# Optimization experiments

Hardware: AMD Instinct MI355X
Metric: run time of the kernel (lower is better)

Reference implementation:

```python
import jax, jax.numpy as jnp
import numpy as np

HEADS = 8
FEATURE = 512
COMPUTE = 256
SEQ = 512
BATCH = 64


def setup_inputs() -> dict:
    key = jax.random.key(0)
    ks = jax.random.split(key, 10)
    d1 = jax.random.normal(ks[0], (BATCH, FEATURE), dtype=jnp.float32)
    d2 = jax.random.normal(ks[1], (SEQ, BATCH, FEATURE), dtype=jnp.float32)
    # linear1: Linear(FEATURE -> COMPUTE) + ReLU
    w1 = jax.random.normal(ks[2], (FEATURE, COMPUTE), dtype=jnp.float32) * (1.0 / np.sqrt(FEATURE))
    b1 = jnp.zeros((COMPUTE,), dtype=jnp.float32)
    # per-head score params, stacked: ws[i] is [2C, C], ps[i] is [C, 1]
    W = jax.random.normal(ks[3], (HEADS, 2 * COMPUTE, COMPUTE), dtype=jnp.float32)
    P = jax.random.normal(ks[4], (HEADS, COMPUTE), dtype=jnp.float32)
    # value projection weight_v: [FEATURE, COMPUTE]
    wv = jax.random.normal(ks[5], (FEATURE, COMPUTE), dtype=jnp.float32)
    # cc: Linear(COMPUTE*HEADS -> 128) + ReLU
    wcc = jax.random.normal(ks[6], (COMPUTE * HEADS, 128), dtype=jnp.float32) * (1.0 / np.sqrt(COMPUTE * HEADS))
    bcc = jnp.zeros((128,), dtype=jnp.float32)
    return {"d1": d1, "d2": d2, "w1": w1, "b1": b1, "W": W, "P": P,
            "wv": wv, "wcc": wcc, "bcc": bcc, "d2_size": SEQ}


def reference(d1, d2, w1, b1, W, P, wv, wcc, bcc, d2_size):
    S, B, F = d2.shape
    # linear1 on flattened d2 rows -> [S*B, C]
    d3 = jax.nn.relu(d2.reshape(-1, F) @ w1 + b1)
    # linear1 on d1, tiled S times along batch axis -> [S*B, C]
    d4 = jax.nn.relu(d1 @ w1 + b1)            # [B, C]
    d4 = jnp.tile(d4, (S, 1))                  # [S*B, C]
    d5 = jnp.concatenate([d3, d4], axis=1).reshape(S, B, -1)  # [S, B, 2C]
    # value path: tanh(d2 @ weight_v) -> [B, S, C]
    tv = jnp.tanh(jnp.einsum('sbf,fc->sbc', d2, wv)).transpose(1, 0, 2)
    # all heads batched: us = tanh(d5 @ W_h) -> [H, S, B, C]
    us = jnp.tanh(jnp.einsum('sbd,hdc->hsbc', d5, W))
    atts = jnp.einsum('hsbc,hc->hbs', us, P)   # [H, B, S]
    scores = jax.nn.softmax(atts, axis=-1)     # softmax over sequence
    vs = jnp.einsum('hbs,bsc->hbc', scores, tv)  # weighted sum over S -> [H, B, C]
    # torch.cat(vs, dim=1): head-major concat -> [B, H*C]
    vs = vs.transpose(1, 0, 2).reshape(B, -1)
    return jax.nn.relu(vs @ wcc + bcc)         # [B, 128]
```

## Files before the change

kernel.cpp:

```cpp
#include <hip/hip_runtime.h>
#include <cstddef>
#include <cstdint>

#define HH 8
#define FF 512
#define CC 256
#define SS 512
#define BB 64
#define SB (SS*BB)

typedef __attribute__((ext_vector_type(4))) float f32x4;
typedef __attribute__((ext_vector_type(8))) short bf16x8;

__device__ __forceinline__ float fast_tanh(float x) {
    float e = __expf(2.0f * x);
    return 1.0f - 2.0f / (e + 1.0f);
}
__device__ __forceinline__ float relu_f(float x) { return fmaxf(x, 0.0f); }

__device__ __forceinline__ unsigned short f2bf(float x) {
    unsigned u = __float_as_uint(x);
    unsigned r = u + 0x7FFFu + ((u >> 16) & 1u);
    return (unsigned short)(r >> 16);
}
__device__ __forceinline__ float bf2f(unsigned short h) {
    return __uint_as_float(((unsigned)h) << 16);
}

__global__ __launch_bounds__(256) void p_prep(
    const float* __restrict__ w1, const float* __restrict__ wv,
    const float* __restrict__ W, const float* __restrict__ d1,
    const float* __restrict__ b1,
    unsigned short* __restrict__ w1t_hi, unsigned short* __restrict__ w1t_lo,
    unsigned short* __restrict__ wvt_hi, unsigned short* __restrict__ wvt_lo,
    unsigned short* __restrict__ Wt_hi, unsigned short* __restrict__ Wt_lo,
    float* __restrict__ d4)
{
    __shared__ float T[64][65];
    __shared__ float As[16][68];
    __shared__ float Bs[16][68];
    const int tid = threadIdx.x;
    const int bid = blockIdx.x;
    if (bid < 192) {
        const float* src;
        unsigned short *dhi, *dlo;
        int K, kt, nt;
        if (bid < 64) {
            int m = bid >> 5;
            int t = bid & 31;
            kt = t >> 2; nt = t & 3; K = FF;
            src = m ? wv : w1;
            dhi = m ? wvt_hi : w1t_hi;
            dlo = m ? wvt_lo : w1t_lo;
        } else {
            int t = bid - 64;
            int h = t >> 4; int tt = t & 15;
            kt = tt >> 2; nt = tt & 3; K = CC;
            src = W + (size_t)h * 2 * CC * CC;
            dhi = Wt_hi + (size_t)h * CC * CC;
            dlo = Wt_lo + (size_t)h * CC * CC;
        }
        const int k0 = kt * 64, n0 = nt * 64;
        #pragma unroll
        for (int jj = 0; jj < 4; ++jj) {
            int i = (tid >> 4) + jj * 16;
            int j = (tid & 15) * 4;
            float4 v = *(const float4*)(src + (size_t)(k0 + i) * CC + n0 + j);
            T[i][j] = v.x; T[i][j+1] = v.y; T[i][j+2] = v.z; T[i][j+3] = v.w;
        }
        __syncthreads();
        #pragma unroll
        for (int jj = 0; jj < 4; ++jj) {
            int n = (tid >> 4) + jj * 16;
            int kq = (tid & 15) * 4;
            unsigned short hv[4], lv[4];
            #pragma unroll
            for (int q = 0; q < 4; ++q) {
                float x = T[kq + q][n];
                unsigned short hx = f2bf(x);
                hv[q] = hx; lv[q] = f2bf(x - bf2f(hx));
            }
            size_t o = (size_t)(n0 + n) * K + k0 + kq;
            *(ushort4*)(dhi + o) = *(ushort4*)hv;
            *(ushort4*)(dlo + o) = *(ushort4*)lv;
        }
    } else {
        const int n0 = (bid - 192) * 64;
        const int tx = tid & 15, ty = tid >> 4;
        const int lm = tid >> 2, lk4 = (tid & 3) * 4;
        const int bk = tid >> 4, bn4 = (tid & 15) * 4;
        float acc[4][4] = {};
        for (int k0 = 0; k0 < FF; k0 += 16) {
            float4 a = *(const float4*)(d1 + (size_t)lm * FF + k0 + lk4);
            As[lk4+0][lm] = a.x; As[lk4+1][lm] = a.y;
            As[lk4+2][lm] = a.z; As[lk4+3][lm] = a.w;
            *(float4*)&Bs[bk][bn4] = *(const float4*)(w1 + (size_t)(k0+bk)*CC + n0 + bn4);
            __syncthreads();
            #pragma unroll
            for (int kk = 0; kk < 16; ++kk) {
                float4 a4 = *(const float4*)&As[kk][ty*4];
                float4 b4 = *(const float4*)&Bs[kk][tx*4];
                float av[4] = {a4.x, a4.y, a4.z, a4.w};
                float bv[4] = {b4.x, b4.y, b4.z, b4.w};
                #pragma unroll
                for (int i = 0; i < 4; ++i)
                    #pragma unroll
                    for (int j = 0; j < 4; ++j)
                        acc[i][j] = fmaf(av[i], bv[j], acc[i][j]);
            }
            __syncthreads();
        }
        #pragma unroll
        for (int i = 0; i < 4; ++i) {
            int row = ty*4 + i;
            #pragma unroll
            for (int j = 0; j < 4; ++j)
                d4[(size_t)row*CC + n0 + tx*4 + j] = relu_f(acc[i][j] + b1[n0 + tx*4 + j]);
        }
    }
}

__global__ __launch_bounds__(256, 2) void k1_main(
    const float* __restrict__ d2,
    const unsigned short* __restrict__ w1t_hi, const unsigned short* __restrict__ w1t_lo,
    const unsigned short* __restrict__ wvt_hi, const unsigned short* __restrict__ wvt_lo,
    const float* __restrict__ b1,
    const float* __restrict__ d4, const float* __restrict__ W,
    unsigned short* __restrict__ d3_hi, unsigned short* __restrict__ d3_lo,
    unsigned short* __restrict__ tv, float* __restrict__ e4)
{
    __shared__ __align__(16) unsigned short A_hi[128][40];
    __shared__ __align__(16) unsigned short A_lo[128][40];
    __shared__ __align__(16) unsigned short B_hi[256][40];
    __shared__ __align__(16) unsigned short B_lo[256][40];

    const int tid = threadIdx.x;
    const int bid = blockIdx.x;

    if (bid >= 512) {
        float (*As)[68] = (float(*)[68])&A_hi[0][0];
        float (*Bs)[68] = (float(*)[68])&A_lo[0][0];
        const int idx = bid - 512;
        const int n0 = (idx & 3) * 64;
        const int h  = idx >> 2;
        const float* Wh = W + ((size_t)h * 2 * CC + CC) * CC;
        const int tx = tid & 15, ty = tid >> 4;
        const int lm = tid >> 2, lk4 = (tid & 3) * 4;
        const int bk = tid >> 4, bn4 = (tid & 15) * 4;
        float acc[4][4] = {};
        for (int k0 = 0; k0 < CC; k0 += 16) {
            float4 a = *(const float4*)(d4 + (size_t)lm * CC + k0 + lk4);
            As[lk4+0][lm] = a.x; As[lk4+1][lm] = a.y;
            As[lk4+2][lm] = a.z; As[lk4+3][lm] = a.w;
            *(float4*)&Bs[bk][bn4] = *(const float4*)(Wh + (size_t)(k0+bk)*CC + n0 + bn4);
            __syncthreads();
            #pragma unroll
            for (int kk = 0; kk < 16; ++kk) {
                float4 a4 = *(const float4*)&As[kk][ty*4];
                float4 b4 = *(const float4*)&Bs[kk][tx*4];
                float av[4] = {a4.x, a4.y, a4.z, a4.w};
                float bv[4] = {b4.x, b4.y, b4.z, b4.w};
                #pragma unroll
                for (int i = 0; i < 4; ++i)
                    #pragma unroll
                    for (int j = 0; j < 4; ++j)
                        acc[i][j] = fmaf(av[i], bv[j], acc[i][j]);
            }
            __syncthreads();
        }
        #pragma unroll
        for (int i = 0; i < 4; ++i) {
            int b = ty*4 + i;
            #pragma unroll
            for (int j = 0; j < 4; ++j)
                e4[((size_t)h*BB + b)*CC + n0 + tx*4 + j] = acc[i][j];
        }
        return;
    }

    const int path = bid >> 8;
    const int r0 = (bid & 255) * 128;
    const int lane = tid & 63, w = tid >> 6;
    const int rowgrp = w & 1, colgrp = w >> 1;
    const int cb = lane & 15, quad = lane >> 4;
    const unsigned short* BH = path ? wvt_hi : w1t_hi;
    const unsigned short* BL = path ? wvt_lo : w1t_lo;

    f32x4 acc[4][8];
    f32x4 zero = {0.0f, 0.0f, 0.0f, 0.0f};
    #pragma unroll
    for (int rt = 0; rt < 4; ++rt)
        #pragma unroll
        for (int ct = 0; ct < 8; ++ct) acc[rt][ct] = zero;

    const int ar = tid >> 1, ak = (tid & 1) * 16;

    for (int k0 = 0; k0 < FF; k0 += 32) {
        {
            const float* src = d2 + (size_t)(r0 + ar) * FF + k0 + ak;
            float v[16];
            *(float4*)&v[0]  = *(const float4*)(src);
            *(float4*)&v[4]  = *(const float4*)(src + 4);
            *(float4*)&v[8]  = *(const float4*)(src + 8);
            *(float4*)&v[12] = *(const float4*)(src + 12);
            bf16x8 vh0, vh1, vl0, vl1;
            #pragma unroll
            for (int j = 0; j < 8; ++j) {
                unsigned short h = f2bf(v[j]);
                vh0[j] = (short)h; vl0[j] = (short)f2bf(v[j] - bf2f(h));
                unsigned short h2 = f2bf(v[j+8]);
                vh1[j] = (short)h2; vl1[j] = (short)f2bf(v[j+8] - bf2f(h2));
            }
            *(bf16x8*)&A_hi[ar][ak]     = vh0;
            *(bf16x8*)&A_hi[ar][ak + 8] = vh1;
            *(bf16x8*)&A_lo[ar][ak]     = vl0;
            *(bf16x8*)&A_lo[ar][ak + 8] = vl1;
        }
        #pragma unroll
        for (int j = 0; j < 4; ++j) {
            int idx = j * 256 + tid;
            int n = idx >> 2, kp = (idx & 3) * 8;
            *(bf16x8*)&B_hi[n][kp] = *(const bf16x8*)(BH + (size_t)n * FF + k0 + kp);
            *(bf16x8*)&B_lo[n][kp] = *(const bf16x8*)(BL + (size_t)n * FF + k0 + kp);
        }
        __syncthreads();
        bf16x8 ahf[4], alf[4];
        #pragma unroll
        for (int rt = 0; rt < 4; ++rt) {
            ahf[rt] = *(bf16x8*)&A_hi[rowgrp*64 + rt*16 + cb][quad*8];
            alf[rt] = *(bf16x8*)&A_lo[rowgrp*64 + rt*16 + cb][quad*8];
        }
        #pragma unroll
        for (int ct = 0; ct < 8; ++ct) {
            bf16x8 bh = *(bf16x8*)&B_hi[colgrp*128 + ct*16 + cb][quad*8];
            bf16x8 bl = *(bf16x8*)&B_lo[colgrp*128 + ct*16 + cb][quad*8];
            #pragma unroll
            for (int rt = 0; rt < 4; ++rt) {
                acc[rt][ct] = __builtin_amdgcn_mfma_f32_16x16x32_bf16(ahf[rt], bh, acc[rt][ct], 0, 0, 0);
                acc[rt][ct] = __builtin_amdgcn_mfma_f32_16x16x32_bf16(ahf[rt], bl, acc[rt][ct], 0, 0, 0);
                acc[rt][ct] = __builtin_amdgcn_mfma_f32_16x16x32_bf16(alf[rt], bh, acc[rt][ct], 0, 0, 0);
            }
        }
        __syncthreads();
    }
    if (path == 0) {
        float bias[8];
        #pragma unroll
        for (int ct = 0; ct < 8; ++ct) bias[ct] = b1[colgrp*128 + ct*16 + cb];
        #pragma unroll
        for (int rt = 0; rt < 4; ++rt) {
            #pragma unroll
            for (int r = 0; r < 4; ++r) {
                int gr = r0 + rowgrp*64 + rt*16 + quad*4 + r;
                #pragma unroll
                for (int ct = 0; ct < 8; ++ct) {
                    int c = colgrp*128 + ct*16 + cb;
                    float val = relu_f(acc[rt][ct][r] + bias[ct]);
                    unsigned short hv = f2bf(val);
                    d3_hi[(size_t)gr * CC + c] = hv;
                    d3_lo[(size_t)gr * CC + c] = f2bf(val - bf2f(hv));
                }
            }
        }
    } else {
        #pragma unroll
        for (int rt = 0; rt < 4; ++rt) {
            #pragma unroll
            for (int r = 0; r < 4; ++r) {
                int gr = r0 + rowgrp*64 + rt*16 + quad*4 + r;
                int s = gr >> 6, b = gr & 63;
                #pragma unroll
                for (int ct = 0; ct < 8; ++ct) {
                    int c = colgrp*128 + ct*16 + cb;
                    tv[((size_t)b * SS + s) * CC + c] = f2bf(fast_tanh(acc[rt][ct][r]));
                }
            }
        }
    }
}

__global__ __launch_bounds__(256, 2) void k3_atts(
    const unsigned short* __restrict__ d3_hi, const unsigned short* __restrict__ d3_lo,
    const unsigned short* __restrict__ Wt_hi, const unsigned short* __restrict__ Wt_lo,
    const float* __restrict__ e4, const float* __restrict__ P,
    float* __restrict__ atts)
{
    __shared__ __align__(16) unsigned short A_hi[128][40];
    __shared__ __align__(16) unsigned short A_lo[128][40];
    __shared__ __align__(16) unsigned short B_hi[256][40];
    __shared__ __align__(16) unsigned short B_lo[256][40];
    __shared__ float red[2][128];

    const int tid = threadIdx.x;
    const int lane = tid & 63, w = tid >> 6;
    const int h = blockIdx.y;
    const int r0 = blockIdx.x * 128;
    const int rowgrp = w & 1, colgrp = w >> 1;
    const int cb = lane & 15, quad = lane >> 4;

    const unsigned short* WhH = Wt_hi + (size_t)h * CC * CC;
    const unsigned short* WhL = Wt_lo + (size_t)h * CC * CC;

    f32x4 acc[4][8];
    f32x4 zero = {0.0f, 0.0f, 0.0f, 0.0f};
    #pragma unroll
    for (int rt = 0; rt < 4; ++rt)
        #pragma unroll
        for (int ct = 0; ct < 8; ++ct) acc[rt][ct] = zero;

    const int ar = tid >> 1, ak = (tid & 1) * 16;

    for (int k0 = 0; k0 < CC; k0 += 32) {
        *(bf16x8*)&A_hi[ar][ak]     = *(const bf16x8*)(d3_hi + (size_t)(r0 + ar) * CC + k0 + ak);
        *(bf16x8*)&A_hi[ar][ak + 8] = *(const bf16x8*)(d3_hi + (size_t)(r0 + ar) * CC + k0 + ak + 8);
        *(bf16x8*)&A_lo[ar][ak]     = *(const bf16x8*)(d3_lo + (size_t)(r0 + ar) * CC + k0 + ak);
        *(bf16x8*)&A_lo[ar][ak + 8] = *(const bf16x8*)(d3_lo + (size_t)(r0 + ar) * CC + k0 + ak + 8);
        #pragma unroll
        for (int j = 0; j < 4; ++j) {
            int idx = j * 256 + tid;
            int n = idx >> 2, kp = (idx & 3) * 8;
            *(bf16x8*)&B_hi[n][kp] = *(const bf16x8*)(WhH + (size_t)n * CC + k0 + kp);
            *(bf16x8*)&B_lo[n][kp] = *(const bf16x8*)(WhL + (size_t)n * CC + k0 + kp);
        }
        __syncthreads();
        bf16x8 ahf[4], alf[4];
        #pragma unroll
        for (int rt = 0; rt < 4; ++rt) {
            ahf[rt] = *(bf16x8*)&A_hi[rowgrp*64 + rt*16 + cb][quad*8];
            alf[rt] = *(bf16x8*)&A_lo[rowgrp*64 + rt*16 + cb][quad*8];
        }
        #pragma unroll
        for (int ct = 0; ct < 8; ++ct) {
            bf16x8 bh = *(bf16x8*)&B_hi[colgrp*128 + ct*16 + cb][quad*8];
            bf16x8 bl = *(bf16x8*)&B_lo[colgrp*128 + ct*16 + cb][quad*8];
            #pragma unroll
            for (int rt = 0; rt < 4; ++rt) {
                acc[rt][ct] = __builtin_amdgcn_mfma_f32_16x16x32_bf16(ahf[rt], bh, acc[rt][ct], 0, 0, 0);
                acc[rt][ct] = __builtin_amdgcn_mfma_f32_16x16x32_bf16(ahf[rt], bl, acc[rt][ct], 0, 0, 0);
                acc[rt][ct] = __builtin_amdgcn_mfma_f32_16x16x32_bf16(alf[rt], bh, acc[rt][ct], 0, 0, 0);
            }
        }
        __syncthreads();
    }
    float Pv[8];
    #pragma unroll
    for (int ct = 0; ct < 8; ++ct) Pv[ct] = P[(size_t)h * CC + colgrp*128 + ct*16 + cb];
    #pragma unroll
    for (int rt = 0; rt < 4; ++rt) {
        #pragma unroll
        for (int r = 0; r < 4; ++r) {
            int b = rt*16 + quad*4 + r;
            const float* e4p = e4 + ((size_t)h * BB + b) * CC + colgrp*128 + cb;
            float part = 0.0f;
            #pragma unroll
            for (int ct = 0; ct < 8; ++ct) {
                float u = acc[rt][ct][r] + e4p[ct*16];
                part = fmaf(Pv[ct], fast_tanh(u), part);
            }
            part += __shfl_xor(part, 1); part += __shfl_xor(part, 2);
            part += __shfl_xor(part, 4); part += __shfl_xor(part, 8);
            if (cb == 0) red[colgrp][rowgrp*64 + b] = part;
        }
    }
    __syncthreads();
    if (tid < 128) {
        float v = red[0][tid] + red[1][tid];
        int gr = r0 + tid;
        int s = gr >> 6, b = gr & 63;
        atts[((size_t)h * BB + b) * SS + s] = v;
    }
}

__global__ __launch_bounds__(256) void k456_out(
    const float* __restrict__ atts, const unsigned short* __restrict__ tv,
    const float* __restrict__ wcc, const float* __restrict__ bcc,
    float* __restrict__ out)
{
    __shared__ float sc[HH][SS];
    __shared__ float red[4][2048];
    const int b = blockIdx.x;
    const int tid = threadIdx.x;
    const int lane = tid & 63, w = tid >> 6;

    for (int i = tid; i < HH*SS; i += 256) {
        int h = i >> 9, s = i & 511;
        sc[h][s] = atts[((size_t)h*BB + b)*SS + s];
    }
    __syncthreads();
    #pragma unroll
    for (int t = 0; t < 2; ++t) {
        int hh = w*2 + t;
        float x[8];
        #pragma unroll
        for (int j = 0; j < 8; ++j) x[j] = sc[hh][j*64 + lane];
        float m = x[0];
        #pragma unroll
        for (int j = 1; j < 8; ++j) m = fmaxf(m, x[j]);
        #pragma unroll
        for (int d = 1; d < 64; d <<= 1) m = fmaxf(m, __shfl_xor(m, d));
        float sum = 0.0f;
        #pragma unroll
        for (int j = 0; j < 8; ++j) { x[j] = __expf(x[j] - m); sum += x[j]; }
        #pragma unroll
        for (int d = 1; d < 64; d <<= 1) sum += __shfl_xor(sum, d);
        float inv = 1.0f / sum;
        #pragma unroll
        for (int j = 0; j < 8; ++j) sc[hh][j*64 + lane] = x[j] * inv;
    }
    __syncthreads();
    {
        const int cl = tid & 63, stripe = tid >> 6;
        const int c0 = cl * 4;
        const unsigned short* tvb = tv + ((size_t)b * SS + stripe * 128) * CC + c0;
        float acc[HH][4] = {};
        for (int si = 0; si < 128; ++si) {
            uint2 u = *(const uint2*)(tvb + (size_t)si * CC);
            float x0 = bf2f((unsigned short)(u.x));
            float x1 = bf2f((unsigned short)(u.x >> 16));
            float x2 = bf2f((unsigned short)(u.y));
            float x3 = bf2f((unsigned short)(u.y >> 16));
            int s = stripe * 128 + si;
            #pragma unroll
            for (int h = 0; h < HH; ++h) {
                float wgt = sc[h][s];
                acc[h][0] = fmaf(wgt, x0, acc[h][0]);
                acc[h][1] = fmaf(wgt, x1, acc[h][1]);
                acc[h][2] = fmaf(wgt, x2, acc[h][2]);
                acc[h][3] = fmaf(wgt, x3, acc[h][3]);
            }
        }
        #pragma unroll
        for (int h = 0; h < HH; ++h)
            #pragma unroll
            for (int j = 0; j < 4; ++j)
                red[stripe][h*256 + c0 + j] = acc[h][j];
    }
    __syncthreads();
    for (int i = tid; i < 2048; i += 256)
        red[0][i] = red[0][i] + red[1][i] + red[2][i] + red[3][i];
    __syncthreads();
    {
        const int n = tid & 127, half = tid >> 7;
        float o = 0.0f;
        const int kbase = half * 1024;
        for (int k = 0; k < 1024; ++k)
            o = fmaf(red[0][kbase + k], wcc[(size_t)(kbase + k) * 128 + n], o);
        float* r2 = &sc[0][0];
        r2[half * 128 + n] = o;
    }
    __syncthreads();
    if (tid < 128)
        out[(size_t)b * 128 + tid] = relu_f(sc[0][tid] + sc[0][128 + tid] + bcc[tid]);
}

extern "C" void kernel_launch(void* const* d_in, const int* in_sizes, int n_in,
                              void* d_out, int out_size, void* d_ws, size_t ws_size,
                              hipStream_t stream)
{
    (void)in_sizes; (void)n_in; (void)out_size; (void)ws_size;
    const float* d1  = (const float*)d_in[0];
    const float* d2  = (const float*)d_in[1];
    const float* w1  = (const float*)d_in[2];
    const float* b1  = (const float*)d_in[3];
    const float* W   = (const float*)d_in[4];
    const float* P   = (const float*)d_in[5];
    const float* wv  = (const float*)d_in[6];
    const float* wcc = (const float*)d_in[7];
    const float* bcc = (const float*)d_in[8];
    float* out = (float*)d_out;

    char* p = (char*)d_ws;
    unsigned short* d3_hi = (unsigned short*)p;  p += (size_t)SB * CC * 2;
    unsigned short* d3_lo = (unsigned short*)p;  p += (size_t)SB * CC * 2;
    unsigned short* tv    = (unsigned short*)p;  p += (size_t)BB * SS * CC * 2;
    unsigned short* w1t_hi = (unsigned short*)p; p += (size_t)CC * FF * 2;
    unsigned short* w1t_lo = (unsigned short*)p; p += (size_t)CC * FF * 2;
    unsigned short* wvt_hi = (unsigned short*)p; p += (size_t)CC * FF * 2;
    unsigned short* wvt_lo = (unsigned short*)p; p += (size_t)CC * FF * 2;
    unsigned short* Wt_hi  = (unsigned short*)p; p += (size_t)HH * CC * CC * 2;
    unsigned short* Wt_lo  = (unsigned short*)p; p += (size_t)HH * CC * CC * 2;
    float* d4   = (float*)p;  p += (size_t)BB * CC * 4;
    float* e4   = (float*)p;  p += (size_t)HH * BB * CC * 4;
    float* atts = (float*)p;  p += (size_t)HH * BB * SS * 4;

    p_prep   <<<dim3(196),       256, 0, stream>>>(w1, wv, W, d1, b1,
                  w1t_hi, w1t_lo, wvt_hi, wvt_lo, Wt_hi, Wt_lo, d4);
    k1_main  <<<dim3(544),       256, 0, stream>>>(d2, w1t_hi, w1t_lo,
                  wvt_hi, wvt_lo, b1, d4, W, d3_hi, d3_lo, tv, e4);
    k3_atts  <<<dim3(256, HH),   256, 0, stream>>>(d3_hi, d3_lo, Wt_hi, Wt_lo,
                  e4, P, atts);
    k456_out <<<dim3(BB),        256, 0, stream>>>(atts, tv, wcc, bcc, out);
}
```

Baseline: 370.2 us.

## Load weight tiles via async global-to-LDS and A fragments directly into registers

In both GEMM kernels the B (weight) tiles are now copied with global_load_lds, which goes straight from global memory into LDS without passing through registers. The LDS rows are unpadded, 32 elements wide. The A operand is no longer staged in LDS: each wave loads its MFMA fragments directly from global memory, and in k1 also converts them to hi/lo bf16 there. This cuts LDS traffic and footprint, and may raise occupancy. The cost is that unpadded B rows can cause LDS bank conflicts on the fragment reads, and A rows are re-read by the two column-group waves.

Result: slower. 406.3 us (+9.7%).

```diff
diff --git a/kernel.cpp b/kernel.cpp
--- a/kernel.cpp
+++ b/kernel.cpp
@@ -25,6 +25,13 @@
 }
 __device__ __forceinline__ float bf2f(unsigned short h) {
     return __uint_as_float(((unsigned)h) << 16);
+}
+
+__device__ __forceinline__ void async16(void* lds, const void* gp) {
+    __builtin_amdgcn_global_load_lds(
+        (const __attribute__((address_space(1))) unsigned int*)gp,
+        (__attribute__((address_space(3))) unsigned int*)lds,
+        16, 0, 0);
 }
 
 __global__ __launch_bounds__(256) void p_prep(
@@ -129,17 +136,15 @@
     unsigned short* __restrict__ d3_hi, unsigned short* __restrict__ d3_lo,
     unsigned short* __restrict__ tv, float* __restrict__ e4)
 {
-    __shared__ __align__(16) unsigned short A_hi[128][40];
-    __shared__ __align__(16) unsigned short A_lo[128][40];
-    __shared__ __align__(16) unsigned short B_hi[256][40];
-    __shared__ __align__(16) unsigned short B_lo[256][40];
+    __shared__ __align__(16) unsigned short B_hi[256][32];
+    __shared__ __align__(16) unsigned short B_lo[256][32];
+    __shared__ float As[16][68];
+    __shared__ float Bs[16][68];
 
     const int tid = threadIdx.x;
     const int bid = blockIdx.x;
 
     if (bid >= 512) {
-        float (*As)[68] = (float(*)[68])&A_hi[0][0];
-        float (*Bs)[68] = (float(*)[68])&A_lo[0][0];
         const int idx = bid - 512;
         const int n0 = (idx & 3) * 64;
         const int h  = idx >> 2;
@@ -186,6 +191,9 @@
     const unsigned short* BH = path ? wvt_hi : w1t_hi;
     const unsigned short* BL = path ? wvt_lo : w1t_lo;
 
+    const int dn = w * 64 + (lane >> 2);
+    const int dk = (lane & 3) * 8;
+
     f32x4 acc[4][8];
     f32x4 zero = {0.0f, 0.0f, 0.0f, 0.0f};
     #pragma unroll
@@ -193,43 +201,28 @@
         #pragma unroll
         for (int ct = 0; ct < 8; ++ct) acc[rt][ct] = zero;
 
-    const int ar = tid >> 1, ak = (tid & 1) * 16;
-
     for (int k0 = 0; k0 < FF; k0 += 32) {
-        {
-            const float* src = d2 + (size_t)(r0 + ar) * FF + k0 + ak;
-            float v[16];
-            *(float4*)&v[0]  = *(const float4*)(src);
-            *(float4*)&v[4]  = *(const float4*)(src + 4);
-            *(float4*)&v[8]  = *(const float4*)(src + 8);
-            *(float4*)&v[12] = *(const float4*)(src + 12);
-            bf16x8 vh0, vh1, vl0, vl1;
+        #pragma unroll
+        for (int jj = 0; jj < 4; ++jj) {
+            const size_t go = (size_t)(dn + jj*16) * FF + k0 + dk;
+            async16((char*)B_hi + (w*4 + jj) * 1024, BH + go);
+            async16((char*)B_lo + (w*4 + jj) * 1024, BL + go);
+        }
+        bf16x8 ahf[4], alf[4];
+        #pragma unroll
+        for (int rt = 0; rt < 4; ++rt) {
+            const float* ap = d2 + (size_t)(r0 + rowgrp*64 + rt*16 + cb) * FF + k0 + quad*8;
+            float v[8];
+            *(float4*)&v[0] = *(const float4*)ap;
+            *(float4*)&v[4] = *(const float4*)(ap + 4);
             #pragma unroll
             for (int j = 0; j < 8; ++j) {
                 unsigned short h = f2bf(v[j]);
-                vh0[j] = (short)h; vl0[j] = (short)f2bf(v[j] - bf2f(h));
-                unsigned short h2 = f2bf(v[j+8]);
-                vh1[j] = (short)h2; vl1[j] = (short)f2bf(v[j+8] - bf2f(h2));
-            }
-            *(bf16x8*)&A_hi[ar][ak]     = vh0;
-            *(bf16x8*)&A_hi[ar][ak + 8] = vh1;
-            *(bf16x8*)&A_lo[ar][ak]     = vl0;
-            *(bf16x8*)&A_lo[ar][ak + 8] = vl1;
-        }
-        #pragma unroll
-        for (int j = 0; j < 4; ++j) {
-            int idx = j * 256 + tid;
-            int n = idx >> 2, kp = (idx & 3) * 8;
-            *(bf16x8*)&B_hi[n][kp] = *(const bf16x8*)(BH + (size_t)n * FF + k0 + kp);
-            *(bf16x8*)&B_lo[n][kp] = *(const bf16x8*)(BL + (size_t)n * FF + k0 + kp);
+                ahf[rt][j] = (short)h;
+                alf[rt][j] = (short)f2bf(v[j] - bf2f(h));
+            }
         }
         __syncthreads();
-        bf16x8 ahf[4], alf[4];
-        #pragma unroll
-        for (int rt = 0; rt < 4; ++rt) {
-            ahf[rt] = *(bf16x8*)&A_hi[rowgrp*64 + rt*16 + cb][quad*8];
-            alf[rt] = *(bf16x8*)&A_lo[rowgrp*64 + rt*16 + cb][quad*8];
-        }
         #pragma unroll
         for (int ct = 0; ct < 8; ++ct) {
             bf16x8 bh = *(bf16x8*)&B_hi[colgrp*128 + ct*16 + cb][quad*8];
@@ -285,10 +278,8 @@
     const float* __restrict__ e4, const float* __restrict__ P,
     float* __restrict__ atts)
 {
-    __shared__ __align__(16) unsigned short A_hi[128][40];
-    __shared__ __align__(16) unsigned short A_lo[128][40];
-    __shared__ __align__(16) unsigned short B_hi[256][40];
-    __shared__ __align__(16) unsigned short B_lo[256][40];
+    __shared__ __align__(16) unsigned short B_hi[256][32];
+    __shared__ __align__(16) unsigned short B_lo[256][32];
     __shared__ float red[2][128];
 
     const int tid = threadIdx.x;
@@ -301,6 +292,9 @@
     const unsigned short* WhH = Wt_hi + (size_t)h * CC * CC;
     const unsigned short* WhL = Wt_lo + (size_t)h * CC * CC;
 
+    const int dn = w * 64 + (lane >> 2);
+    const int dk = (lane & 3) * 8;
+
     f32x4 acc[4][8];
     f32x4 zero = {0.0f, 0.0f, 0.0f, 0.0f};
     #pragma unroll
@@ -308,27 +302,21 @@
         #pragma unroll
         for (int ct = 0; ct < 8; ++ct) acc[rt][ct] = zero;
 
-    const int ar = tid >> 1, ak = (tid & 1) * 16;
-
     for (int k0 = 0; k0 < CC; k0 += 32) {
-        *(bf16x8*)&A_hi[ar][ak]     = *(const bf16x8*)(d3_hi + (size_t)(r0 + ar) * CC + k0 + ak);
-        *(bf16x8*)&A_hi[ar][ak + 8] = *(const bf16x8*)(d3_hi + (size_t)(r0 + ar) * CC + k0 + ak + 8);
-        *(bf16x8*)&A_lo[ar][ak]     = *(const bf16x8*)(d3_lo + (size_t)(r0 + ar) * CC + k0 + ak);
-        *(bf16x8*)&A_lo[ar][ak + 8] = *(const bf16x8*)(d3_lo + (size_t)(r0 + ar) * CC + k0 + ak + 8);
-        #pragma unroll
-        for (int j = 0; j < 4; ++j) {
-            int idx = j * 256 + tid;
-            int n = idx >> 2, kp = (idx & 3) * 8;
-            *(bf16x8*)&B_hi[n][kp] = *(const bf16x8*)(WhH + (size_t)n * CC + k0 + kp);
-            *(bf16x8*)&B_lo[n][kp] = *(const bf16x8*)(WhL + (size_t)n * CC + k0 + kp);
+        #pragma unroll
+        for (int jj = 0; jj < 4; ++jj) {
+            const size_t go = (size_t)(dn + jj*16) * CC + k0 + dk;
+            async16((char*)B_hi + (w*4 + jj) * 1024, WhH + go);
+            async16((char*)B_lo + (w*4 + jj) * 1024, WhL + go);
+        }
+        bf16x8 ahf[4], alf[4];
+        #pragma unroll
+        for (int rt = 0; rt < 4; ++rt) {
+            const size_t ao = (size_t)(r0 + rowgrp*64 + rt*16 + cb) * CC + k0 + quad*8;
+            ahf[rt] = *(const bf16x8*)(d3_hi + ao);
+            alf[rt] = *(const bf16x8*)(d3_lo + ao);
         }
         __syncthreads();
-        bf16x8 ahf[4], alf[4];
-        #pragma unroll
-        for (int rt = 0; rt < 4; ++rt) {
-            ahf[rt] = *(bf16x8*)&A_hi[rowgrp*64 + rt*16 + cb][quad*8];
-            alf[rt] = *(bf16x8*)&A_lo[rowgrp*64 + rt*16 + cb][quad*8];
-        }
         #pragma unroll
         for (int ct = 0; ct < 8; ++ct) {
             bf16x8 bh = *(bf16x8*)&B_hi[colgrp*128 + ct*16 + cb][quad*8];
```

## Split GEMM output columns into halves, accumulate scores atomically, widen final kernel

Applied to the files above, without the earlier changes.

k1_main and k3_atts now use 128x128 output tiles instead of 128x256, doubling the block count and raising the occupancy hint to 3. The aim is more parallelism and lower per-block register and LDS pressure. Because each k3_atts block now holds only half the columns, its partial attention scores are combined with atomicAdd, and p_prep gains extra blocks that zero the atts buffer first. k456_out moves to 512 threads with 8 sequence stripes to shorten its serial loops. The cost is that the A operands (d2 with its bf16 hi/lo split, and d3) are loaded and converted twice as often, and the atomics add some overhead.

Measured after the change: 379.4 us. +2.5%, slower.

```diff
diff --git a/kernel.cpp b/kernel.cpp
--- a/kernel.cpp
+++ b/kernel.cpp
@@ -34,13 +34,18 @@
     unsigned short* __restrict__ w1t_hi, unsigned short* __restrict__ w1t_lo,
     unsigned short* __restrict__ wvt_hi, unsigned short* __restrict__ wvt_lo,
     unsigned short* __restrict__ Wt_hi, unsigned short* __restrict__ Wt_lo,
-    float* __restrict__ d4)
+    float* __restrict__ d4, float* __restrict__ atts)
 {
     __shared__ float T[64][65];
     __shared__ float As[16][68];
     __shared__ float Bs[16][68];
     const int tid = threadIdx.x;
     const int bid = blockIdx.x;
+    if (bid >= 196) {
+        f32x4 z = {0.0f, 0.0f, 0.0f, 0.0f};
+        *(f32x4*)(atts + (size_t)(bid - 196) * 1024 + tid * 4) = z;
+        return;
+    }
     if (bid < 192) {
         const float* src;
         unsigned short *dhi, *dlo;
@@ -120,7 +125,7 @@
     }
 }
 
-__global__ __launch_bounds__(256, 2) void k1_main(
+__global__ __launch_bounds__(256, 3) void k1_main(
     const float* __restrict__ d2,
     const unsigned short* __restrict__ w1t_hi, const unsigned short* __restrict__ w1t_lo,
     const unsigned short* __restrict__ wvt_hi, const unsigned short* __restrict__ wvt_lo,
@@ -131,16 +136,16 @@
 {
     __shared__ __align__(16) unsigned short A_hi[128][40];
     __shared__ __align__(16) unsigned short A_lo[128][40];
-    __shared__ __align__(16) unsigned short B_hi[256][40];
-    __shared__ __align__(16) unsigned short B_lo[256][40];
+    __shared__ __align__(16) unsigned short B_hi[128][40];
+    __shared__ __align__(16) unsigned short B_lo[128][40];
 
     const int tid = threadIdx.x;
     const int bid = blockIdx.x;
 
-    if (bid >= 512) {
+    if (bid >= 1024) {
         float (*As)[68] = (float(*)[68])&A_hi[0][0];
         float (*Bs)[68] = (float(*)[68])&A_lo[0][0];
-        const int idx = bid - 512;
+        const int idx = bid - 1024;
         const int n0 = (idx & 3) * 64;
         const int h  = idx >> 2;
         const float* Wh = W + ((size_t)h * 2 * CC + CC) * CC;
@@ -178,26 +183,30 @@
         return;
     }
 
-    const int path = bid >> 8;
-    const int r0 = (bid & 255) * 128;
+    const int rowtile = bid & 255;
+    const int colhalf = (bid >> 8) & 1;
+    const int path    = bid >> 9;
+    const int r0 = rowtile * 128;
+    const int n0 = colhalf * 128;
     const int lane = tid & 63, w = tid >> 6;
     const int rowgrp = w & 1, colgrp = w >> 1;
     const int cb = lane & 15, quad = lane >> 4;
     const unsigned short* BH = path ? wvt_hi : w1t_hi;
     const unsigned short* BL = path ? wvt_lo : w1t_lo;
 
-    f32x4 acc[4][8];
+    const int srow = tid >> 1;
+    const int sk   = (tid & 1) * 16;
+
+    f32x4 acc[4][4];
     f32x4 zero = {0.0f, 0.0f, 0.0f, 0.0f};
     #pragma unroll
     for (int rt = 0; rt < 4; ++rt)
         #pragma unroll
-        for (int ct = 0; ct < 8; ++ct) acc[rt][ct] = zero;
-
-    const int ar = tid >> 1, ak = (tid & 1) * 16;
+        for (int ct = 0; ct < 4; ++ct) acc[rt][ct] = zero;
 
     for (int k0 = 0; k0 < FF; k0 += 32) {
         {
-            const float* src = d2 + (size_t)(r0 + ar) * FF + k0 + ak;
+            const float* src = d2 + (size_t)(r0 + srow) * FF + k0 + sk;
             float v[16];
             *(float4*)&v[0]  = *(const float4*)(src);
             *(float4*)&v[4]  = *(const float4*)(src + 4);
@@ -211,17 +220,17 @@
                 unsigned short h2 = f2bf(v[j+8]);
                 vh1[j] = (short)h2; vl1[j] = (short)f2bf(v[j+8] - bf2f(h2));
             }
-            *(bf16x8*)&A_hi[ar][ak]     = vh0;
-            *(bf16x8*)&A_hi[ar][ak + 8] = vh1;
-            *(bf16x8*)&A_lo[ar][ak]     = vl0;
-            *(bf16x8*)&A_lo[ar][ak + 8] = vl1;
-        }
-        #pragma unroll
-        for (int j = 0; j < 4; ++j) {
-            int idx = j * 256 + tid;
-            int n = idx >> 2, kp = (idx & 3) * 8;
-            *(bf16x8*)&B_hi[n][kp] = *(const bf16x8*)(BH + (size_t)n * FF + k0 + kp);
-            *(bf16x8*)&B_lo[n][kp] = *(const bf16x8*)(BL + (size_t)n * FF + k0 + kp);
+            *(bf16x8*)&A_hi[srow][sk]     = vh0;
+            *(bf16x8*)&A_hi[srow][sk + 8] = vh1;
+            *(bf16x8*)&A_lo[srow][sk]     = vl0;
+            *(bf16x8*)&A_lo[srow][sk + 8] = vl1;
+        }
+        {
+            const size_t go = (size_t)(n0 + srow) * FF + k0 + sk;
+            *(bf16x8*)&B_hi[srow][sk]     = *(const bf16x8*)(BH + go);
+            *(bf16x8*)&B_hi[srow][sk + 8] = *(const bf16x8*)(BH + go + 8);
+            *(bf16x8*)&B_lo[srow][sk]     = *(const bf16x8*)(BL + go);
+            *(bf16x8*)&B_lo[srow][sk + 8] = *(const bf16x8*)(BL + go + 8);
         }
         __syncthreads();
         bf16x8 ahf[4], alf[4];
@@ -231,9 +240,9 @@
             alf[rt] = *(bf16x8*)&A_lo[rowgrp*64 + rt*16 + cb][quad*8];
         }
         #pragma unroll
-        for (int ct = 0; ct < 8; ++ct) {
-            bf16x8 bh = *(bf16x8*)&B_hi[colgrp*128 + ct*16 + cb][quad*8];
-            bf16x8 bl = *(bf16x8*)&B_lo[colgrp*128 + ct*16 + cb][quad*8];
+        for (int ct = 0; ct < 4; ++ct) {
+            bf16x8 bh = *(bf16x8*)&B_hi[colgrp*64 + ct*16 + cb][quad*8];
+            bf16x8 bl = *(bf16x8*)&B_lo[colgrp*64 + ct*16 + cb][quad*8];
             #pragma unroll
             for (int rt = 0; rt < 4; ++rt) {
                 acc[rt][ct] = __builtin_amdgcn_mfma_f32_16x16x32_bf16(ahf[rt], bh, acc[rt][ct], 0, 0, 0);
@@ -244,17 +253,17 @@
         __syncthreads();
     }
     if (path == 0) {
-        float bias[8];
-        #pragma unroll
-        for (int ct = 0; ct < 8; ++ct) bias[ct] = b1[colgrp*128 + ct*16 + cb];
+        float bias[4];
+        #pragma unroll
+        for (int ct = 0; ct < 4; ++ct) bias[ct] = b1[n0 + colgrp*64 + ct*16 + cb];
         #pragma unroll
         for (int rt = 0; rt < 4; ++rt) {
             #pragma unroll
             for (int r = 0; r < 4; ++r) {
                 int gr = r0 + rowgrp*64 + rt*16 + quad*4 + r;
                 #pragma unroll
-                for (int ct = 0; ct < 8; ++ct) {
-                    int c = colgrp*128 + ct*16 + cb;
+                for (int ct = 0; ct < 4; ++ct) {
+                    int c = n0 + colgrp*64 + ct*16 + cb;
                     float val = relu_f(acc[rt][ct][r] + bias[ct]);
                     unsigned short hv = f2bf(val);
                     d3_hi[(size_t)gr * CC + c] = hv;
@@ -270,8 +279,8 @@
                 int gr = r0 + rowgrp*64 + rt*16 + quad*4 + r;
                 int s = gr >> 6, b = gr & 63;
                 #pragma unroll
-                for (int ct = 0; ct < 8; ++ct) {
-                    int c = colgrp*128 + ct*16 + cb;
+                for (int ct = 0; ct < 4; ++ct) {
+                    int c = n0 + colgrp*64 + ct*16 + cb;
                     tv[((size_t)b * SS + s) * CC + c] = f2bf(fast_tanh(acc[rt][ct][r]));
                 }
             }
@@ -279,7 +288,7 @@
     }
 }
 
-__global__ __launch_bounds__(256, 2) void k3_atts(
+__global__ __launch_bounds__(256, 3) void k3_atts(
     const unsigned short* __restrict__ d3_hi, const unsigned short* __restrict__ d3_lo,
     const unsigned short* __restrict__ Wt_hi, const unsigned short* __restrict__ Wt_lo,
     const float* __restrict__ e4, const float* __restrict__ P,
@@ -287,40 +296,45 @@
 {
     __shared__ __align__(16) unsigned short A_hi[128][40];
     __shared__ __align__(16) unsigned short A_lo[128][40];
-    __shared__ __align__(16) unsigned short B_hi[256][40];
-    __shared__ __align__(16) unsigned short B_lo[256][40];
+    __shared__ __align__(16) unsigned short B_hi[128][40];
+    __shared__ __align__(16) unsigned short B_lo[128][40];
     __shared__ float red[2][128];
 
     const int tid = threadIdx.x;
     const int lane = tid & 63, w = tid >> 6;
     const int h = blockIdx.y;
-    const int r0 = blockIdx.x * 128;
+    const int rowtile = blockIdx.x & 255;
+    const int colhalf = blockIdx.x >> 8;
+    const int r0 = rowtile * 128;
+    const int n0 = colhalf * 128;
     const int rowgrp = w & 1, colgrp = w >> 1;
     const int cb = lane & 15, quad = lane >> 4;
 
     const unsigned short* WhH = Wt_hi + (size_t)h * CC * CC;
     const unsigned short* WhL = Wt_lo + (size_t)h * CC * CC;
 
-    f32x4 acc[4][8];
+    const int srow = tid >> 1;
+    const int sk   = (tid & 1) * 16;
+
+    f32x4 acc[4][4];
     f32x4 zero = {0.0f, 0.0f, 0.0f, 0.0f};
     #pragma unroll
     for (int rt = 0; rt < 4; ++rt)
         #pragma unroll
-        for (int ct = 0; ct < 8; ++ct) acc[rt][ct] = zero;
-
-    const int ar = tid >> 1, ak = (tid & 1) * 16;
+        for (int ct = 0; ct < 4; ++ct) acc[rt][ct] = zero;
 
     for (int k0 = 0; k0 < CC; k0 += 32) {
-        *(bf16x8*)&A_hi[ar][ak]     = *(const bf16x8*)(d3_hi + (size_t)(r0 + ar) * CC + k0 + ak);
-        *(bf16x8*)&A_hi[ar][ak + 8] = *(const bf16x8*)(d3_hi + (size_t)(r0 + ar) * CC + k0 + ak + 8);
-        *(bf16x8*)&A_lo[ar][ak]     = *(const bf16x8*)(d3_lo + (size_t)(r0 + ar) * CC + k0 + ak);
-        *(bf16x8*)&A_lo[ar][ak + 8] = *(const bf16x8*)(d3_lo + (size_t)(r0 + ar) * CC + k0 + ak + 8);
-        #pragma unroll
-        for (int j = 0; j < 4; ++j) {
-            int idx = j * 256 + tid;
-            int n = idx >> 2, kp = (idx & 3) * 8;
-            *(bf16x8*)&B_hi[n][kp] = *(const bf16x8*)(WhH + (size_t)n * CC + k0 + kp);
-            *(bf16x8*)&B_lo[n][kp] = *(const bf16x8*)(WhL + (size_t)n * CC + k0 + kp);
+        {
+            const size_t ao = (size_t)(r0 + srow) * CC + k0 + sk;
+            *(bf16x8*)&A_hi[srow][sk]     = *(const bf16x8*)(d3_hi + ao);
+            *(bf16x8*)&A_hi[srow][sk + 8] = *(const bf16x8*)(d3_hi + ao + 8);
+            *(bf16x8*)&A_lo[srow][sk]     = *(const bf16x8*)(d3_lo + ao);
+            *(bf16x8*)&A_lo[srow][sk + 8] = *(const bf16x8*)(d3_lo + ao + 8);
+            const size_t go = (size_t)(n0 + srow) * CC + k0 + sk;
+            *(bf16x8*)&B_hi[srow][sk]     = *(const bf16x8*)(WhH + go);
+            *(bf16x8*)&B_hi[srow][sk + 8] = *(const bf16x8*)(WhH + go + 8);
+            *(bf16x8*)&B_lo[srow][sk]     = *(const bf16x8*)(WhL + go);
+            *(bf16x8*)&B_lo[srow][sk + 8] = *(const bf16x8*)(WhL + go + 8);
         }
         __syncthreads();
         bf16x8 ahf[4], alf[4];
@@ -330,9 +344,9 @@
             alf[rt] = *(bf16x8*)&A_lo[rowgrp*64 + rt*16 + cb][quad*8];
         }
         #pragma unroll
-        for (int ct = 0; ct < 8; ++ct) {
-            bf16x8 bh = *(bf16x8*)&B_hi[colgrp*128 + ct*16 + cb][quad*8];
-            bf16x8 bl = *(bf16x8*)&B_lo[colgrp*128 + ct*16 + cb][quad*8];
+        for (int ct = 0; ct < 4; ++ct) {
+            bf16x8 bh = *(bf16x8*)&B_hi[colgrp*64 + ct*16 + cb][quad*8];
+            bf16x8 bl = *(bf16x8*)&B_lo[colgrp*64 + ct*16 + cb][quad*8];
             #pragma unroll
             for (int rt = 0; rt < 4; ++rt) {
                 acc[rt][ct] = __builtin_amdgcn_mfma_f32_16x16x32_bf16(ahf[rt], bh, acc[rt][ct], 0, 0, 0);
@@ -342,24 +356,25 @@
         }
         __syncthreads();
     }
-    float Pv[8];
+    float Pv[4];
     #pragma unroll
-    for (int ct = 0; ct < 8; ++ct) Pv[ct] = P[(size_t)h * CC + colgrp*128 + ct*16 + cb];
+    for (int ct = 0; ct < 4; ++ct) Pv[ct] = P[(size_t)h * CC + n0 + colgrp*64 + ct*16 + cb];
     #pragma unroll
     for (int rt = 0; rt < 4; ++rt) {
         #pragma unroll
         for (int r = 0; r < 4; ++r) {
-            int b = rt*16 + quad*4 + r;
-            const float* e4p = e4 + ((size_t)h * BB + b) * CC + colgrp*128 + cb;
+            int lrow = rt*16 + quad*4 + r;
+            int b = lrow;
+            const float* e4p = e4 + ((size_t)h * BB + b) * CC + n0 + colgrp*64 + cb;
             float part = 0.0f;
             #pragma unroll
-            for (int ct = 0; ct < 8; ++ct) {
+            for (int ct = 0; ct < 4; ++ct) {
                 float u = acc[rt][ct][r] + e4p[ct*16];
                 part = fmaf(Pv[ct], fast_tanh(u), part);
             }
             part += __shfl_xor(part, 1); part += __shfl_xor(part, 2);
             part += __shfl_xor(part, 4); part += __shfl_xor(part, 8);
-            if (cb == 0) red[colgrp][rowgrp*64 + b] = part;
+            if (cb == 0) red[colgrp][rowgrp*64 + lrow] = part;
         }
     }
     __syncthreads();
@@ -367,32 +382,30 @@
         float v = red[0][tid] + red[1][tid];
         int gr = r0 + tid;
         int s = gr >> 6, b = gr & 63;
-        atts[((size_t)h * BB + b) * SS + s] = v;
-    }
-}
-
-__global__ __launch_bounds__(256) void k456_out(
+        atomicAdd(&atts[((size_t)h * BB + b) * SS + s], v);
+    }
+}
+
+__global__ __launch_bounds__(512) void k456_out(
     const float* __restrict__ atts, const unsigned short* __restrict__ tv,
     const float* __restrict__ wcc, const float* __restrict__ bcc,
     float* __restrict__ out)
 {
     __shared__ float sc[HH][SS];
-    __shared__ float red[4][2048];
+    __shared__ float red[8][2048];
     const int b = blockIdx.x;
     const int tid = threadIdx.x;
     const int lane = tid & 63, w = tid >> 6;
 
-    for (int i = tid; i < HH*SS; i += 256) {
+    for (int i = tid; i < HH*SS; i += 512) {
         int h = i >> 9, s = i & 511;
         sc[h][s] = atts[((size_t)h*BB + b)*SS + s];
     }
     __syncthreads();
-    #pragma unroll
-    for (int t = 0; t < 2; ++t) {
-        int hh = w*2 + t;
+    {
         float x[8];
         #pragma unroll
-        for (int j = 0; j < 8; ++j) x[j] = sc[hh][j*64 + lane];
+        for (int j = 0; j < 8; ++j) x[j] = sc[w][j*64 + lane];
         float m = x[0];
         #pragma unroll
         for (int j = 1; j < 8; ++j) m = fmaxf(m, x[j]);
@@ -405,21 +418,21 @@
         for (int d = 1; d < 64; d <<= 1) sum += __shfl_xor(sum, d);
         float inv = 1.0f / sum;
         #pragma unroll
-        for (int j = 0; j < 8; ++j) sc[hh][j*64 + lane] = x[j] * inv;
+        for (int j = 0; j < 8; ++j) sc[w][j*64 + lane] = x[j] * inv;
     }
     __syncthreads();
     {
         const int cl = tid & 63, stripe = tid >> 6;
         const int c0 = cl * 4;
-        const unsigned short* tvb = tv + ((size_t)b * SS + stripe * 128) * CC + c0;
+        const unsigned short* tvb = tv + ((size_t)b * SS + stripe * 64) * CC + c0;
         float acc[HH][4] = {};
-        for (int si = 0; si < 128; ++si) {
+        for (int si = 0; si < 64; ++si) {
             uint2 u = *(const uint2*)(tvb + (size_t)si * CC);
             float x0 = bf2f((unsigned short)(u.x));
             float x1 = bf2f((unsigned short)(u.x >> 16));
             float x2 = bf2f((unsigned short)(u.y));
             float x3 = bf2f((unsigned short)(u.y >> 16));
-            int s = stripe * 128 + si;
+            int s = stripe * 64 + si;
             #pragma unroll
             for (int h = 0; h < HH; ++h) {
                 float wgt = sc[h][s];
@@ -436,21 +449,28 @@
                 red[stripe][h*256 + c0 + j] = acc[h][j];
     }
     __syncthreads();
-    for (int i = tid; i < 2048; i += 256)
-        red[0][i] = red[0][i] + red[1][i] + red[2][i] + red[3][i];
+    for (int i = tid; i < 2048; i += 512) {
+        float v = red[0][i];
+        #pragma unroll
+        for (int st = 1; st < 8; ++st) v += red[st][i];
+        red[0][i] = v;
+    }
     __syncthreads();
     {
-        const int n = tid & 127, half = tid >> 7;
+        const int n = tid & 127, q = tid >> 7;
         float o = 0.0f;
-        const int kbase = half * 1024;
-        for (int k = 0; k < 1024; ++k)
+        const int kbase = q * 512;
+        for (int k = 0; k < 512; ++k)
             o = fmaf(red[0][kbase + k], wcc[(size_t)(kbase + k) * 128 + n], o);
         float* r2 = &sc[0][0];
-        r2[half * 128 + n] = o;
+        r2[q * 128 + n] = o;
     }
     __syncthreads();
-    if (tid < 128)
-        out[(size_t)b * 128 + tid] = relu_f(sc[0][tid] + sc[0][128 + tid] + bcc[tid]);
+    if (tid < 128) {
+        float* r2 = &sc[0][0];
+        out[(size_t)b * 128 + tid] =
+            relu_f(r2[tid] + r2[128 + tid] + r2[256 + tid] + r2[384 + tid] + bcc[tid]);
+    }
 }
 
 extern "C" void kernel_launch(void* const* d_in, const int* in_sizes, int n_in,
@@ -483,11 +503,11 @@
     float* e4   = (float*)p;  p += (size_t)HH * BB * CC * 4;
     float* atts = (float*)p;  p += (size_t)HH * BB * SS * 4;
 
-    p_prep   <<<dim3(196),       256, 0, stream>>>(w1, wv, W, d1, b1,
-                  w1t_hi, w1t_lo, wvt_hi, wvt_lo, Wt_hi, Wt_lo, d4);
-    k1_main  <<<dim3(544),       256, 0, stream>>>(d2, w1t_hi, w1t_lo,
+    p_prep   <<<dim3(452),       256, 0, stream>>>(w1, wv, W, d1, b1,
+                  w1t_hi, w1t_lo, wvt_hi, wvt_lo, Wt_hi, Wt_lo, d4, atts);
+    k1_main  <<<dim3(1056),      256, 0, stream>>>(d2, w1t_hi, w1t_lo,
                   wvt_hi, wvt_lo, b1, d4, W, d3_hi, d3_lo, tv, e4);
-    k3_atts  <<<dim3(256, HH),   256, 0, stream>>>(d3_hi, d3_lo, Wt_hi, Wt_lo,
+    k3_atts  <<<dim3(512, HH),   256, 0, stream>>>(d3_hi, d3_lo, Wt_hi, Wt_lo,
                   e4, P, atts);
-    k456_out <<<dim3(BB),        256, 0, stream>>>(atts, tv, wcc, bcc, out);
-}
+    k456_out <<<dim3(BB),        512, 0, stream>>>(atts, tv, wcc, bcc, out);
+}
```
